# Optimization experiments

Measured on AMD Instinct MI355X. Metric: run time of the kernel, lower is better.

Reference implementation:

```python
import jax, jax.numpy as jnp
import numpy as np
from jax import lax

PATCH = 11          # patch_size
DIL = 2             # dilation_patch
PAD = (PATCH // 2) * DIL  # 10
EPS = 1e-5


def setup_inputs() -> dict:
    key = jax.random.key(0)
    k0, k1, kw, kb, kg, kbe = jax.random.split(key, 6)
    B, C, H, W = 8, 128, 192, 192
    x0 = jax.random.normal(k0, (B, C, H, W), dtype=jnp.float32)
    x1 = jax.random.normal(k1, (B, C, H, W), dtype=jnp.float32)
    # Conv2d(121, 8, k=3, s=1, p=1) params + BatchNorm2d(8) affine params
    conv_w = jax.random.normal(kw, (8, 121, 3, 3), dtype=jnp.float32) * 0.05
    conv_b = jax.random.normal(kb, (8,), dtype=jnp.float32) * 0.05
    gamma = jnp.ones((8,), dtype=jnp.float32)
    beta = jnp.zeros((8,), dtype=jnp.float32)
    return {"x0": x0, "x1": x1, "conv_w": conv_w, "conv_b": conv_b,
            "gamma": gamma, "beta": beta}


def _correlation(x0, x1):
    """spatial_correlation_sample(kernel=1, patch=11, stride=1, pad=0, dil_patch=2).
    out[b, pi*11+pj, i, j] = sum_c x0[b,c,i,j] * x1[b,c, i+(pi-5)*2, j+(pj-5)*2]
    (zero-padded outside)."""
    x1p = jnp.pad(x1, ((0, 0), (0, 0), (PAD, PAD), (PAD, PAD)))
    slices = []
    for pi in range(PATCH):       # static 11x11 displacement grid
        for pj in range(PATCH):
            x1s = lax.dynamic_slice(x1p, (0, 0, pi * DIL, pj * DIL), x1.shape)
            slices.append(jnp.einsum('bchw,bchw->bhw', x0, x1s))
    return jnp.stack(slices, axis=1)  # [B, 121, H, W]


def reference(x0, x1, conv_w, conv_b, gamma, beta):
    y = _correlation(x0, x1)  # [B, 121, H, W]
    y = lax.conv_general_dilated(y, conv_w, window_strides=(1, 1),
                                 padding=((1, 1), (1, 1)),
                                 dimension_numbers=('NCHW', 'OIHW', 'NCHW'))
    y = y + conv_b[None, :, None, None]
    # BatchNorm2d in training mode: batch statistics over (B, H, W), biased var
    mean = jnp.mean(y, axis=(0, 2, 3))
    var = jnp.var(y, axis=(0, 2, 3))
    y = (y - mean[None, :, None, None]) * (gamma / jnp.sqrt(var + EPS))[None, :, None, None] \
        + beta[None, :, None, None]
    return jax.nn.relu(y)
```

## Files before the change

kernel.cpp:

```cpp
#include <hip/hip_runtime.h>

#define HH 192
#define WW 192
#define CC 128
#define BB 8
#define HW (HH * WW)
#define OC 8
#define NPIX (BB * HW)

typedef __attribute__((ext_vector_type(8))) short bf16x8;
typedef __attribute__((ext_vector_type(4))) float f32x4;

__device__ __forceinline__ unsigned short f2bf(float f) {
    unsigned int u = __float_as_uint(f);
    u += 0x7fffu + ((u >> 16) & 1u);
    return (unsigned short)(u >> 16);
}
__device__ __forceinline__ float bf2f(unsigned short u) {
    return __uint_as_float(((unsigned int)u) << 16);
}

__global__ __launch_bounds__(256) void k_transpose(
    const float* __restrict__ x0, const float* __restrict__ x1,
    unsigned short* __restrict__ ws)
{
    const int h = blockIdx.x, b = blockIdx.y, t = blockIdx.z;
    const float* src = t ? x1 : x0;
    unsigned short* dst = ws + (size_t)t * ((size_t)BB * HH * WW * CC);
    __shared__ unsigned short lds[WW * 130];

    for (int idx = threadIdx.x; idx < CC * WW; idx += 256) {
        const int w = idx % WW, c = idx / WW;
        const float v = src[((size_t)(b * CC + c) * HH + h) * WW + w];
        lds[w * 130 + c] = f2bf(v);
    }
    __syncthreads();
    unsigned int* dw = (unsigned int*)(dst + (size_t)(b * HH + h) * WW * CC);
    for (int idx = threadIdx.x; idx < WW * (CC / 2); idx += 256) {
        const int w = idx / (CC / 2), cp = idx % (CC / 2);
        const unsigned int lo = lds[w * 130 + 2 * cp];
        const unsigned int hi = lds[w * 130 + 2 * cp + 1];
        dw[w * (CC / 2) + cp] = lo | (hi << 16);
    }
}

__global__ __launch_bounds__(384, 3) void k_corr_mfma_conv(
    const unsigned short* __restrict__ x0t, const unsigned short* __restrict__ x1t,
    const float* __restrict__ cw, const float* __restrict__ cb,
    float* __restrict__ y)
{
    const int b    = blockIdx.y;
    const int i0   = blockIdx.x * 6;
    const int tid  = threadIdx.x;
    const int wave = tid >> 6, lane = tid & 63;
    const int ln15 = lane & 15, kg = lane >> 4;

    __shared__ unsigned short corr[8][194][11];

    if (tid < 176) {
        const int ir = tid / 22, rem = tid % 22;
        const int pj = rem % 11, jj = (rem < 11) ? 0 : 193;
        corr[ir][jj][pj] = 0;
    }

    float yacc[3][OC];
#pragma unroll
    for (int k = 0; k < 3; ++k)
#pragma unroll
        for (int o = 0; o < OC; ++o) yacc[k][o] = 0.f;

    const int jt  = tid % 192;
    const int irb = tid / 192;

    const bf16x8 zf = {0,0,0,0,0,0,0,0};

    for (int pi = 0; pi < 11; ++pi) {
        __syncthreads();

        for (int g = wave; g < 96; g += 6) {
            const int ir  = g / 12, rem = g % 12;
            const int par = rem / 6, ut = rem % 6;
            const int u0  = ut * 16;
            const int i   = i0 - 1 + ir;
            const bool iv = (i >= 0) && (i < HH);
            const int r   = i + 2 * pi - 10;
            const bool rv = iv && (r >= 0) && (r < HH);
            const int icl = iv ? i : 0;
            const int rcl = rv ? r : 0;

            const unsigned short* pa =
                x0t + ((size_t)((b * HH + icl) * WW + (2 * (u0 + ln15) + par)) * CC + kg * 8);
            bf16x8 a0, a1, a2, a3;
            if (iv) {
                a0 = *(const bf16x8*)(pa);
                a1 = *(const bf16x8*)(pa + 32);
                a2 = *(const bf16x8*)(pa + 64);
                a3 = *(const bf16x8*)(pa + 96);
            } else { a0 = a1 = a2 = a3 = zf; }

#pragma unroll
            for (int vt = 0; vt < 2; ++vt) {
                const int v0 = u0 - 8 + vt * 16;
                const int v  = v0 + ln15;
                const bool vv = rv && (v >= 0) && (v < 96);
                const int vcl = (v < 0) ? 0 : (v > 95 ? 95 : v);
                const unsigned short* pb =
                    x1t + ((size_t)((b * HH + rcl) * WW + (2 * vcl + par)) * CC + kg * 8);
                bf16x8 b0 = *(const bf16x8*)(pb);
                bf16x8 b1 = *(const bf16x8*)(pb + 32);
                bf16x8 b2 = *(const bf16x8*)(pb + 64);
                bf16x8 b3 = *(const bf16x8*)(pb + 96);
                if (!vv) { b0 = zf; b1 = zf; b2 = zf; b3 = zf; }

                f32x4 c = {0.f, 0.f, 0.f, 0.f};
                c = __builtin_amdgcn_mfma_f32_16x16x32_bf16(a0, b0, c, 0, 0, 0);
                c = __builtin_amdgcn_mfma_f32_16x16x32_bf16(a1, b1, c, 0, 0, 0);
                c = __builtin_amdgcn_mfma_f32_16x16x32_bf16(a2, b2, c, 0, 0, 0);
                c = __builtin_amdgcn_mfma_f32_16x16x32_bf16(a3, b3, c, 0, 0, 0);

#pragma unroll
                for (int reg = 0; reg < 4; ++reg) {
                    const int u  = u0 + kg * 4 + reg;
                    const int pj = v0 + ln15 - u + 5;
                    if (pj >= 0 && pj < 11)
                        corr[ir][2 * u + par + 1][pj] = f2bf(c[reg]);
                }
            }
        }
        __syncthreads();

        for (int ki = 0; ki < 3; ++ki) {
            for (int kj = 0; kj < 3; ++kj) {
                float cv[3][11];
#pragma unroll
                for (int k = 0; k < 3; ++k) {
                    const unsigned short* cp = &corr[irb + 2 * k + ki][jt + kj][0];
#pragma unroll
                    for (int pj = 0; pj < 11; ++pj) cv[k][pj] = bf2f(cp[pj]);
                }
#pragma unroll
                for (int o = 0; o < OC; ++o) {
                    float y0 = yacc[0][o], y1 = yacc[1][o], y2 = yacc[2][o];
#pragma unroll
                    for (int pj = 0; pj < 11; ++pj) {
                        const float wv =
                            cw[(((o * 121) + pi * 11 + pj) * 3 + ki) * 3 + kj];
                        y0 = fmaf(wv, cv[0][pj], y0);
                        y1 = fmaf(wv, cv[1][pj], y1);
                        y2 = fmaf(wv, cv[2][pj], y2);
                    }
                    yacc[0][o] = y0; yacc[1][o] = y1; yacc[2][o] = y2;
                }
            }
        }
    }

#pragma unroll
    for (int k = 0; k < 3; ++k) {
        const int irow = i0 + irb + 2 * k;
#pragma unroll
        for (int o = 0; o < OC; ++o)
            y[((size_t)(b * OC + o) * HH + irow) * WW + jt] = yacc[k][o] + cb[o];
    }
}

__global__ __launch_bounds__(256) void k_corr_conv(
    const float* __restrict__ x0, const float* __restrict__ x1,
    const float* __restrict__ cw, const float* __restrict__ cb,
    float* __restrict__ y)
{
    const int b  = blockIdx.z;
    const int i0 = blockIdx.y * 14;
    const int j0 = blockIdx.x * 14;
    const int li = threadIdx.x >> 4;
    const int lj = threadIdx.x & 15;
    const int gi = i0 + li - 1;
    const int gj = j0 + lj - 1;
    const bool valid    = (gi >= 0) & (gi < HH) & (gj >= 0) & (gj < WW);
    const bool interior = (li >= 1) & (li <= 14) & (lj >= 1) & (lj <= 14)
                        & (gi < HH) & (gj < WW);

    __shared__ float corr[16][16][13];

    float yacc[OC];
#pragma unroll
    for (int o = 0; o < OC; ++o) yacc[o] = 0.f;

    const size_t bbase = (size_t)b * CC * HW;
    const float* x0p = x0 + bbase + (size_t)gi * WW + gj;

    for (int pi = 0; pi < 11; ++pi) {
        float acc[11];
#pragma unroll
        for (int k = 0; k < 11; ++k) acc[k] = 0.f;

        const int r = gi + 2 * pi - 10;
        if (valid && r >= 0 && r < HH) {
            const float* p0 = x0p;
            if (gj >= 10 && gj <= WW - 11) {
                const float* p1o = x1 + bbase + (size_t)r * WW + (gj - 10);
#pragma unroll 2
                for (int c = 0; c < CC; ++c) {
                    const float a = *p0;
#pragma unroll
                    for (int k = 0; k < 11; ++k)
                        acc[k] = fmaf(a, p1o[2 * k], acc[k]);
                    p0 += HW; p1o += HW;
                }
            } else {
                const float* p1 = x1 + bbase + (size_t)r * WW;
#pragma unroll 2
                for (int c = 0; c < CC; ++c) {
                    const float a = *p0;
#pragma unroll
                    for (int k = 0; k < 11; ++k) {
                        const int col = gj + 2 * k - 10;
                        const float v = (col >= 0 && col < WW) ? p1[col] : 0.f;
                        acc[k] = fmaf(a, v, acc[k]);
                    }
                    p0 += HW; p1 += HW;
                }
            }
        }

        __syncthreads();
#pragma unroll
        for (int k = 0; k < 11; ++k) corr[li][lj][k] = acc[k];
        __syncthreads();

        if (interior) {
#pragma unroll
            for (int ki = 0; ki < 3; ++ki) {
#pragma unroll
                for (int kj = 0; kj < 3; ++kj) {
                    float cv[11];
#pragma unroll
                    for (int k = 0; k < 11; ++k)
                        cv[k] = corr[li + ki - 1][lj + kj - 1][k];
#pragma unroll
                    for (int o = 0; o < OC; ++o) {
#pragma unroll
                        for (int k = 0; k < 11; ++k) {
                            const float wv =
                                cw[(((o * 121) + pi * 11 + k) * 3 + ki) * 3 + kj];
                            yacc[o] = fmaf(wv, cv[k], yacc[o]);
                        }
                    }
                }
            }
        }
    }

    if (interior) {
#pragma unroll
        for (int o = 0; o < OC; ++o)
            y[(size_t)(b * OC + o) * HW + (size_t)gi * WW + gj] = yacc[o] + cb[o];
    }
}

__global__ __launch_bounds__(256) void k_stats_partial(
    const float* __restrict__ y, float* __restrict__ ws)
{
    const int o = blockIdx.x & 7;
    const int b = blockIdx.x >> 3;
    const float4* p = (const float4*)(y + (size_t)(b * OC + o) * HW);
    float s = 0.f, q = 0.f;
    for (int t = threadIdx.x; t < HW / 4; t += 256) {
        const float4 v = p[t];
        s += v.x + v.y + v.z + v.w;
        q = fmaf(v.x, v.x, q); q = fmaf(v.y, v.y, q);
        q = fmaf(v.z, v.z, q); q = fmaf(v.w, v.w, q);
    }
#pragma unroll
    for (int off = 32; off > 0; off >>= 1) {
        s += __shfl_down(s, off);
        q += __shfl_down(q, off);
    }
    __shared__ float ss[4], sq[4];
    const int lane = threadIdx.x & 63, wv = threadIdx.x >> 6;
    if (lane == 0) { ss[wv] = s; sq[wv] = q; }
    __syncthreads();
    if (threadIdx.x == 0) {
        ws[blockIdx.x]      = ss[0] + ss[1] + ss[2] + ss[3];
        ws[64 + blockIdx.x] = sq[0] + sq[1] + sq[2] + sq[3];
    }
}

__global__ void k_stats_final(float* __restrict__ ws,
                              const float* __restrict__ gamma,
                              const float* __restrict__ beta)
{
    const int o = threadIdx.x;
    if (o < 8) {
        float S = 0.f, Q = 0.f;
#pragma unroll
        for (int b = 0; b < 8; ++b) {
            S += ws[b * 8 + o];
            Q += ws[64 + b * 8 + o];
        }
        const float invN = 1.f / (float)NPIX;
        const float mean = S * invN;
        const float var  = Q * invN - mean * mean;
        const float sc   = gamma[o] / sqrtf(var + 1e-5f);
        ws[128 + o] = sc;
        ws[136 + o] = beta[o] - mean * sc;
    }
}

__global__ __launch_bounds__(256) void k_bn_relu(
    float* __restrict__ y, const float* __restrict__ ws)
{
    const int i = blockIdx.x * 256 + threadIdx.x;
    const int o = (i / (HW / 4)) & 7;
    const float sc = ws[128 + o], sh = ws[136 + o];
    float4 v = ((float4*)y)[i];
    v.x = fmaxf(fmaf(v.x, sc, sh), 0.f);
    v.y = fmaxf(fmaf(v.y, sc, sh), 0.f);
    v.z = fmaxf(fmaf(v.z, sc, sh), 0.f);
    v.w = fmaxf(fmaf(v.w, sc, sh), 0.f);
    ((float4*)y)[i] = v;
}

extern "C" void kernel_launch(void* const* d_in, const int* in_sizes, int n_in,
                              void* d_out, int out_size, void* d_ws, size_t ws_size,
                              hipStream_t stream)
{
    const float* x0    = (const float*)d_in[0];
    const float* x1    = (const float*)d_in[1];
    const float* cw    = (const float*)d_in[2];
    const float* cb    = (const float*)d_in[3];
    const float* gamma = (const float*)d_in[4];
    const float* beta  = (const float*)d_in[5];
    float* y  = (float*)d_out;
    float* ws = (float*)d_ws;

    const size_t need = (size_t)2 * BB * HH * WW * CC * sizeof(unsigned short);

    if (ws_size >= need) {
        unsigned short* x0t = (unsigned short*)d_ws;
        unsigned short* x1t = x0t + (size_t)BB * HH * WW * CC;
        k_transpose<<<dim3(HH, BB, 2), 256, 0, stream>>>(x0, x1, (unsigned short*)d_ws);
        k_corr_mfma_conv<<<dim3(32, BB), 384, 0, stream>>>(x0t, x1t, cw, cb, y);
    } else {
        dim3 g1(14, 14, 8);
        k_corr_conv<<<g1, 256, 0, stream>>>(x0, x1, cw, cb, y);
    }
    k_stats_partial<<<64, 256, 0, stream>>>(y, ws);
    k_stats_final<<<1, 64, 0, stream>>>(ws, gamma, beta);
    k_bn_relu<<<(OC * BB * HW / 4) / 256, 256, 0, stream>>>(y, ws);
}
```

Before: 611.7 us.

## Shrink correlation-conv tiles to two output rows per block and keep fp32 LDS

The fused correlation+conv kernel now has each block produce 2 output rows instead of 6, giving 768 blocks interleaved across batch instead of 256. The LDS correlation buffer is stored as fp32 rather than bf16, and out-of-range rows and columns are zeroed at the LDS store instead of on the loaded operands, so loads are clamped and unconditional. The aim is better CU occupancy and fewer idle waves, at the cost of more halo recomputation: 4 correlation rows are computed per 2 output rows, versus 8 per 6 before.

```diff
diff --git a/kernel.cpp b/kernel.cpp
--- a/kernel.cpp
+++ b/kernel.cpp
@@ -16,9 +16,6 @@
     u += 0x7fffu + ((u >> 16) & 1u);
     return (unsigned short)(u >> 16);
 }
-__device__ __forceinline__ float bf2f(unsigned short u) {
-    return __uint_as_float(((unsigned int)u) << 16);
-}
 
 __global__ __launch_bounds__(256) void k_transpose(
     const float* __restrict__ x0, const float* __restrict__ x1,
@@ -49,68 +46,59 @@
     const float* __restrict__ cw, const float* __restrict__ cb,
     float* __restrict__ y)
 {
-    const int b    = blockIdx.y;
-    const int i0   = blockIdx.x * 6;
+    const int bid  = blockIdx.x;
+    const int b    = bid & 7;
+    const int i0   = (bid >> 3) * 2;
     const int tid  = threadIdx.x;
     const int wave = tid >> 6, lane = tid & 63;
     const int ln15 = lane & 15, kg = lane >> 4;
 
-    __shared__ unsigned short corr[8][194][11];
-
-    if (tid < 176) {
+    __shared__ float corr[4][194][11];
+
+    if (tid < 88) {
         const int ir = tid / 22, rem = tid % 22;
         const int pj = rem % 11, jj = (rem < 11) ? 0 : 193;
-        corr[ir][jj][pj] = 0;
-    }
-
-    float yacc[3][OC];
-#pragma unroll
-    for (int k = 0; k < 3; ++k)
-#pragma unroll
-        for (int o = 0; o < OC; ++o) yacc[k][o] = 0.f;
-
-    const int jt  = tid % 192;
-    const int irb = tid / 192;
-
-    const bf16x8 zf = {0,0,0,0,0,0,0,0};
+        corr[ir][jj][pj] = 0.f;
+    }
+
+    float yacc[OC];
+#pragma unroll
+    for (int o = 0; o < OC; ++o) yacc[o] = 0.f;
+
+    const int oi = tid / 192;
+    const int jt = tid % 192;
 
     for (int pi = 0; pi < 11; ++pi) {
         __syncthreads();
 
-        for (int g = wave; g < 96; g += 6) {
+        for (int g = wave; g < 48; g += 6) {
             const int ir  = g / 12, rem = g % 12;
             const int par = rem / 6, ut = rem % 6;
             const int u0  = ut * 16;
             const int i   = i0 - 1 + ir;
-            const bool iv = (i >= 0) && (i < HH);
             const int r   = i + 2 * pi - 10;
-            const bool rv = iv && (r >= 0) && (r < HH);
-            const int icl = iv ? i : 0;
-            const int rcl = rv ? r : 0;
+            const bool gv = (i >= 0) && (i < HH) && (r >= 0) && (r < HH);
+            const int icl = min(max(i, 0), HH - 1);
+            const int rcl = min(max(r, 0), HH - 1);
 
             const unsigned short* pa =
                 x0t + ((size_t)((b * HH + icl) * WW + (2 * (u0 + ln15) + par)) * CC + kg * 8);
-            bf16x8 a0, a1, a2, a3;
-            if (iv) {
-                a0 = *(const bf16x8*)(pa);
-                a1 = *(const bf16x8*)(pa + 32);
-                a2 = *(const bf16x8*)(pa + 64);
-                a3 = *(const bf16x8*)(pa + 96);
-            } else { a0 = a1 = a2 = a3 = zf; }
+            const bf16x8 a0 = *(const bf16x8*)(pa);
+            const bf16x8 a1 = *(const bf16x8*)(pa + 32);
+            const bf16x8 a2 = *(const bf16x8*)(pa + 64);
+            const bf16x8 a3 = *(const bf16x8*)(pa + 96);
 
 #pragma unroll
             for (int vt = 0; vt < 2; ++vt) {
-                const int v0 = u0 - 8 + vt * 16;
-                const int v  = v0 + ln15;
-                const bool vv = rv && (v >= 0) && (v < 96);
-                const int vcl = (v < 0) ? 0 : (v > 95 ? 95 : v);
+                const int v0  = u0 - 8 + vt * 16;
+                const int v   = v0 + ln15;
+                const int vcl = min(max(v, 0), 95);
                 const unsigned short* pb =
                     x1t + ((size_t)((b * HH + rcl) * WW + (2 * vcl + par)) * CC + kg * 8);
-                bf16x8 b0 = *(const bf16x8*)(pb);
-                bf16x8 b1 = *(const bf16x8*)(pb + 32);
-                bf16x8 b2 = *(const bf16x8*)(pb + 64);
-                bf16x8 b3 = *(const bf16x8*)(pb + 96);
-                if (!vv) { b0 = zf; b1 = zf; b2 = zf; b3 = zf; }
+                const bf16x8 b0 = *(const bf16x8*)(pb);
+                const bf16x8 b1 = *(const bf16x8*)(pb + 32);
+                const bf16x8 b2 = *(const bf16x8*)(pb + 64);
+                const bf16x8 b3 = *(const bf16x8*)(pb + 96);
 
                 f32x4 c = {0.f, 0.f, 0.f, 0.f};
                 c = __builtin_amdgcn_mfma_f32_16x16x32_bf16(a0, b0, c, 0, 0, 0);
@@ -118,12 +106,13 @@
                 c = __builtin_amdgcn_mfma_f32_16x16x32_bf16(a2, b2, c, 0, 0, 0);
                 c = __builtin_amdgcn_mfma_f32_16x16x32_bf16(a3, b3, c, 0, 0, 0);
 
+                const bool lv = gv && (v >= 0) && (v < 96);
 #pragma unroll
                 for (int reg = 0; reg < 4; ++reg) {
                     const int u  = u0 + kg * 4 + reg;
-                    const int pj = v0 + ln15 - u + 5;
+                    const int pj = v - u + 5;
                     if (pj >= 0 && pj < 11)
-                        corr[ir][2 * u + par + 1][pj] = f2bf(c[reg]);
+                        corr[ir][2 * u + par + 1][pj] = lv ? c[reg] : 0.f;
                 }
             }
         }
@@ -131,37 +120,29 @@
 
         for (int ki = 0; ki < 3; ++ki) {
             for (int kj = 0; kj < 3; ++kj) {
-                float cv[3][11];
-#pragma unroll
-                for (int k = 0; k < 3; ++k) {
-                    const unsigned short* cp = &corr[irb + 2 * k + ki][jt + kj][0];
-#pragma unroll
-                    for (int pj = 0; pj < 11; ++pj) cv[k][pj] = bf2f(cp[pj]);
-                }
+                const float* cp = &corr[oi + ki][jt + kj][0];
+                float cv[11];
+#pragma unroll
+                for (int pj = 0; pj < 11; ++pj) cv[pj] = cp[pj];
 #pragma unroll
                 for (int o = 0; o < OC; ++o) {
-                    float y0 = yacc[0][o], y1 = yacc[1][o], y2 = yacc[2][o];
+                    float acc = yacc[o];
 #pragma unroll
                     for (int pj = 0; pj < 11; ++pj) {
                         const float wv =
                             cw[(((o * 121) + pi * 11 + pj) * 3 + ki) * 3 + kj];
-                        y0 = fmaf(wv, cv[0][pj], y0);
-                        y1 = fmaf(wv, cv[1][pj], y1);
-                        y2 = fmaf(wv, cv[2][pj], y2);
+                        acc = fmaf(wv, cv[pj], acc);
                     }
-                    yacc[0][o] = y0; yacc[1][o] = y1; yacc[2][o] = y2;
+                    yacc[o] = acc;
                 }
             }
         }
     }
 
-#pragma unroll
-    for (int k = 0; k < 3; ++k) {
-        const int irow = i0 + irb + 2 * k;
-#pragma unroll
-        for (int o = 0; o < OC; ++o)
-            y[((size_t)(b * OC + o) * HH + irow) * WW + jt] = yacc[k][o] + cb[o];
-    }
+    const int irow = i0 + oi;
+#pragma unroll
+    for (int o = 0; o < OC; ++o)
+        y[((size_t)(b * OC + o) * HH + irow) * WW + jt] = yacc[o] + cb[o];
 }
 
 __global__ __launch_bounds__(256) void k_corr_conv(
@@ -340,7 +321,7 @@
         unsigned short* x0t = (unsigned short*)d_ws;
         unsigned short* x1t = x0t + (size_t)BB * HH * WW * CC;
         k_transpose<<<dim3(HH, BB, 2), 256, 0, stream>>>(x0, x1, (unsigned short*)d_ws);
-        k_corr_mfma_conv<<<dim3(32, BB), 384, 0, stream>>>(x0t, x1t, cw, cb, y);
+        k_corr_mfma_conv<<<768, 384, 0, stream>>>(x0t, x1t, cw, cb, y);
     } else {
         dim3 g1(14, 14, 8);
         k_corr_conv<<<g1, 256, 0, stream>>>(x0, x1, cw, cb, y);
```

Result: slower. 706.7 us (+15.5%).

## Software-pipeline MFMA fragment loads and store correlation tile in fp32 LDS

Applied to the files above, without the earlier changes.

Restructures the correlation stage so each wave owns a fixed column tile and double-buffers its bf16 fragment loads, prefetching the next row/parity (and next pi) while issuing MFMAs for the current one. Boundary handling moves from zeroing loaded fragments to masking the stored results. The LDS correlation tile becomes fp32, which removes bf16 round-trips but doubles LDS use and may reduce resident blocks per CU. The batch-norm stats reduction is also split over four times as many blocks.

```diff
diff --git a/kernel.cpp b/kernel.cpp
--- a/kernel.cpp
+++ b/kernel.cpp
@@ -16,9 +16,6 @@
     u += 0x7fffu + ((u >> 16) & 1u);
     return (unsigned short)(u >> 16);
 }
-__device__ __forceinline__ float bf2f(unsigned short u) {
-    return __uint_as_float(((unsigned int)u) << 16);
-}
 
 __global__ __launch_bounds__(256) void k_transpose(
     const float* __restrict__ x0, const float* __restrict__ x1,
@@ -44,6 +41,67 @@
     }
 }
 
+__device__ __forceinline__ void load_frags(
+    bf16x8 (&fa)[4], bf16x8 (&fb)[2][4],
+    const unsigned short* __restrict__ x0b, const unsigned short* __restrict__ x1b,
+    int i0, int u0, int ln15, int kg, int pi, int s)
+{
+    const int ir = s >> 1, par = s & 1;
+    const int i  = i0 - 1 + ir;
+    const int r  = i + 2 * pi - 10;
+    const int icl = min(max(i, 0), HH - 1);
+    const int rcl = min(max(r, 0), HH - 1);
+
+    const unsigned short* pa =
+        x0b + ((size_t)(icl * WW + (2 * (u0 + ln15) + par))) * CC + kg * 8;
+    fa[0] = *(const bf16x8*)(pa);
+    fa[1] = *(const bf16x8*)(pa + 32);
+    fa[2] = *(const bf16x8*)(pa + 64);
+    fa[3] = *(const bf16x8*)(pa + 96);
+
+#pragma unroll
+    for (int vt = 0; vt < 2; ++vt) {
+        const int v   = u0 - 8 + vt * 16 + ln15;
+        const int vcl = min(max(v, 0), 95);
+        const unsigned short* pb =
+            x1b + ((size_t)(rcl * WW + (2 * vcl + par))) * CC + kg * 8;
+        fb[vt][0] = *(const bf16x8*)(pb);
+        fb[vt][1] = *(const bf16x8*)(pb + 32);
+        fb[vt][2] = *(const bf16x8*)(pb + 64);
+        fb[vt][3] = *(const bf16x8*)(pb + 96);
+    }
+}
+
+__device__ __forceinline__ void consume_frags(
+    const bf16x8 (&fa)[4], const bf16x8 (&fb)[2][4],
+    float (&corr)[8][194][11],
+    int i0, int u0, int ln15, int kg, int pi, int s)
+{
+    const int ir = s >> 1, par = s & 1;
+    const int i  = i0 - 1 + ir;
+    const int r  = i + 2 * pi - 10;
+    const bool gv = (i >= 0) && (i < HH) && (r >= 0) && (r < HH);
+
+#pragma unroll
+    for (int vt = 0; vt < 2; ++vt) {
+        f32x4 c = {0.f, 0.f, 0.f, 0.f};
+        c = __builtin_amdgcn_mfma_f32_16x16x32_bf16(fa[0], fb[vt][0], c, 0, 0, 0);
+        c = __builtin_amdgcn_mfma_f32_16x16x32_bf16(fa[1], fb[vt][1], c, 0, 0, 0);
+        c = __builtin_amdgcn_mfma_f32_16x16x32_bf16(fa[2], fb[vt][2], c, 0, 0, 0);
+        c = __builtin_amdgcn_mfma_f32_16x16x32_bf16(fa[3], fb[vt][3], c, 0, 0, 0);
+
+        const int v  = u0 - 8 + vt * 16 + ln15;
+        const bool lv = gv && (v >= 0) && (v < 96);
+#pragma unroll
+        for (int rg = 0; rg < 4; ++rg) {
+            const int u  = u0 + kg * 4 + rg;
+            const int pj = v - u + 5;
+            if (pj >= 0 && pj < 11)
+                corr[ir][2 * u + par + 1][pj] = lv ? c[rg] : 0.f;
+        }
+    }
+}
+
 __global__ __launch_bounds__(384, 3) void k_corr_mfma_conv(
     const unsigned short* __restrict__ x0t, const unsigned short* __restrict__ x1t,
     const float* __restrict__ cw, const float* __restrict__ cb,
@@ -54,13 +112,14 @@
     const int tid  = threadIdx.x;
     const int wave = tid >> 6, lane = tid & 63;
     const int ln15 = lane & 15, kg = lane >> 4;
-
-    __shared__ unsigned short corr[8][194][11];
+    const int u0   = wave * 16;
+
+    __shared__ float corr[8][194][11];
 
     if (tid < 176) {
         const int ir = tid / 22, rem = tid % 22;
         const int pj = rem % 11, jj = (rem < 11) ? 0 : 193;
-        corr[ir][jj][pj] = 0;
+        corr[ir][jj][pj] = 0.f;
     }
 
     float yacc[3][OC];
@@ -72,60 +131,27 @@
     const int jt  = tid % 192;
     const int irb = tid / 192;
 
-    const bf16x8 zf = {0,0,0,0,0,0,0,0};
+    const size_t ibase = (size_t)b * HH * WW * CC;
+    const unsigned short* x0b = x0t + ibase;
+    const unsigned short* x1b = x1t + ibase;
+
+    bf16x8 fa0[4], fa1[4];
+    bf16x8 fb0[2][4], fb1[2][4];
+
+    load_frags(fa0, fb0, x0b, x1b, i0, u0, ln15, kg, 0, 0);
 
     for (int pi = 0; pi < 11; ++pi) {
         __syncthreads();
 
-        for (int g = wave; g < 96; g += 6) {
-            const int ir  = g / 12, rem = g % 12;
-            const int par = rem / 6, ut = rem % 6;
-            const int u0  = ut * 16;
-            const int i   = i0 - 1 + ir;
-            const bool iv = (i >= 0) && (i < HH);
-            const int r   = i + 2 * pi - 10;
-            const bool rv = iv && (r >= 0) && (r < HH);
-            const int icl = iv ? i : 0;
-            const int rcl = rv ? r : 0;
-
-            const unsigned short* pa =
-                x0t + ((size_t)((b * HH + icl) * WW + (2 * (u0 + ln15) + par)) * CC + kg * 8);
-            bf16x8 a0, a1, a2, a3;
-            if (iv) {
-                a0 = *(const bf16x8*)(pa);
-                a1 = *(const bf16x8*)(pa + 32);
-                a2 = *(const bf16x8*)(pa + 64);
-                a3 = *(const bf16x8*)(pa + 96);
-            } else { a0 = a1 = a2 = a3 = zf; }
-
-#pragma unroll
-            for (int vt = 0; vt < 2; ++vt) {
-                const int v0 = u0 - 8 + vt * 16;
-                const int v  = v0 + ln15;
-                const bool vv = rv && (v >= 0) && (v < 96);
-                const int vcl = (v < 0) ? 0 : (v > 95 ? 95 : v);
-                const unsigned short* pb =
-                    x1t + ((size_t)((b * HH + rcl) * WW + (2 * vcl + par)) * CC + kg * 8);
-                bf16x8 b0 = *(const bf16x8*)(pb);
-                bf16x8 b1 = *(const bf16x8*)(pb + 32);
-                bf16x8 b2 = *(const bf16x8*)(pb + 64);
-                bf16x8 b3 = *(const bf16x8*)(pb + 96);
-                if (!vv) { b0 = zf; b1 = zf; b2 = zf; b3 = zf; }
-
-                f32x4 c = {0.f, 0.f, 0.f, 0.f};
-                c = __builtin_amdgcn_mfma_f32_16x16x32_bf16(a0, b0, c, 0, 0, 0);
-                c = __builtin_amdgcn_mfma_f32_16x16x32_bf16(a1, b1, c, 0, 0, 0);
-                c = __builtin_amdgcn_mfma_f32_16x16x32_bf16(a2, b2, c, 0, 0, 0);
-                c = __builtin_amdgcn_mfma_f32_16x16x32_bf16(a3, b3, c, 0, 0, 0);
-
-#pragma unroll
-                for (int reg = 0; reg < 4; ++reg) {
-                    const int u  = u0 + kg * 4 + reg;
-                    const int pj = v0 + ln15 - u + 5;
-                    if (pj >= 0 && pj < 11)
-                        corr[ir][2 * u + par + 1][pj] = f2bf(c[reg]);
-                }
-            }
+#pragma unroll
+        for (int sp = 0; sp < 8; ++sp) {
+            const int s0 = 2 * sp, s1 = 2 * sp + 1;
+            load_frags(fa1, fb1, x0b, x1b, i0, u0, ln15, kg, pi, s1);
+            consume_frags(fa0, fb0, corr, i0, u0, ln15, kg, pi, s0);
+            const int pin = (sp == 7) ? min(pi + 1, 10) : pi;
+            const int s2  = (sp == 7) ? 0 : s1 + 1;
+            load_frags(fa0, fb0, x0b, x1b, i0, u0, ln15, kg, pin, s2);
+            consume_frags(fa1, fb1, corr, i0, u0, ln15, kg, pi, s1);
         }
         __syncthreads();
 
@@ -134,9 +160,9 @@
                 float cv[3][11];
 #pragma unroll
                 for (int k = 0; k < 3; ++k) {
-                    const unsigned short* cp = &corr[irb + 2 * k + ki][jt + kj][0];
-#pragma unroll
-                    for (int pj = 0; pj < 11; ++pj) cv[k][pj] = bf2f(cp[pj]);
+                    const float* cp = &corr[irb + 2 * k + ki][jt + kj][0];
+#pragma unroll
+                    for (int pj = 0; pj < 11; ++pj) cv[k][pj] = cp[pj];
                 }
 #pragma unroll
                 for (int o = 0; o < OC; ++o) {
@@ -144,7 +170,7 @@
 #pragma unroll
                     for (int pj = 0; pj < 11; ++pj) {
                         const float wv =
-                            cw[(((o * 121) + pi * 11 + pj) * 3 + ki) * 3 + kj];
+                            cw[o * 1089 + (pi * 11 + pj) * 9 + ki * 3 + kj];
                         y0 = fmaf(wv, cv[0][pj], y0);
                         y1 = fmaf(wv, cv[1][pj], y1);
                         y2 = fmaf(wv, cv[2][pj], y2);
@@ -261,28 +287,29 @@
 __global__ __launch_bounds__(256) void k_stats_partial(
     const float* __restrict__ y, float* __restrict__ ws)
 {
-    const int o = blockIdx.x & 7;
-    const int b = blockIdx.x >> 3;
-    const float4* p = (const float4*)(y + (size_t)(b * OC + o) * HW);
-    float s = 0.f, q = 0.f;
-    for (int t = threadIdx.x; t < HW / 4; t += 256) {
+    const int bid = blockIdx.x;
+    const int b = bid >> 5, rem = bid & 31;
+    const int o = rem >> 2, q = rem & 3;
+    const float4* p = (const float4*)(y + (size_t)(b * OC + o) * HW) + q * (HW / 16);
+    float s = 0.f, qq = 0.f;
+    for (int t = threadIdx.x; t < HW / 16; t += 256) {
         const float4 v = p[t];
         s += v.x + v.y + v.z + v.w;
-        q = fmaf(v.x, v.x, q); q = fmaf(v.y, v.y, q);
-        q = fmaf(v.z, v.z, q); q = fmaf(v.w, v.w, q);
+        qq = fmaf(v.x, v.x, qq); qq = fmaf(v.y, v.y, qq);
+        qq = fmaf(v.z, v.z, qq); qq = fmaf(v.w, v.w, qq);
     }
 #pragma unroll
     for (int off = 32; off > 0; off >>= 1) {
-        s += __shfl_down(s, off);
-        q += __shfl_down(q, off);
+        s  += __shfl_down(s, off);
+        qq += __shfl_down(qq, off);
     }
     __shared__ float ss[4], sq[4];
     const int lane = threadIdx.x & 63, wv = threadIdx.x >> 6;
-    if (lane == 0) { ss[wv] = s; sq[wv] = q; }
+    if (lane == 0) { ss[wv] = s; sq[wv] = qq; }
     __syncthreads();
     if (threadIdx.x == 0) {
-        ws[blockIdx.x]      = ss[0] + ss[1] + ss[2] + ss[3];
-        ws[64 + blockIdx.x] = sq[0] + sq[1] + sq[2] + sq[3];
+        ws[bid]       = ss[0] + ss[1] + ss[2] + ss[3];
+        ws[256 + bid] = sq[0] + sq[1] + sq[2] + sq[3];
     }
 }
 
@@ -294,16 +321,18 @@
     if (o < 8) {
         float S = 0.f, Q = 0.f;
 #pragma unroll
-        for (int b = 0; b < 8; ++b) {
-            S += ws[b * 8 + o];
-            Q += ws[64 + b * 8 + o];
-        }
+        for (int b = 0; b < 8; ++b)
+#pragma unroll
+            for (int q = 0; q < 4; ++q) {
+                S += ws[b * 32 + o * 4 + q];
+                Q += ws[256 + b * 32 + o * 4 + q];
+            }
         const float invN = 1.f / (float)NPIX;
         const float mean = S * invN;
         const float var  = Q * invN - mean * mean;
         const float sc   = gamma[o] / sqrtf(var + 1e-5f);
-        ws[128 + o] = sc;
-        ws[136 + o] = beta[o] - mean * sc;
+        ws[512 + o] = sc;
+        ws[520 + o] = beta[o] - mean * sc;
     }
 }
 
@@ -312,7 +341,7 @@
 {
     const int i = blockIdx.x * 256 + threadIdx.x;
     const int o = (i / (HW / 4)) & 7;
-    const float sc = ws[128 + o], sh = ws[136 + o];
+    const float sc = ws[512 + o], sh = ws[520 + o];
     float4 v = ((float4*)y)[i];
     v.x = fmaxf(fmaf(v.x, sc, sh), 0.f);
     v.y = fmaxf(fmaf(v.y, sc, sh), 0.f);
@@ -345,7 +374,7 @@
         dim3 g1(14, 14, 8);
         k_corr_conv<<<g1, 256, 0, stream>>>(x0, x1, cw, cb, y);
     }
-    k_stats_partial<<<64, 256, 0, stream>>>(y, ws);
+    k_stats_partial<<<256, 256, 0, stream>>>(y, ws);
     k_stats_final<<<1, 64, 0, stream>>>(ws, gamma, beta);
     k_bn_relu<<<(OC * BB * HW / 4) / 256, 256, 0, stream>>>(y, ws);
 }
```

New measurement: 804.9 us. +31.6%, slower.

## Split correlation-conv kernel over displacement rows into partial sums for more blocks

Applied to the files above, without the earlier changes.

The fused correlation+conv kernel now divides the 11 displacement rows (pi) across up to four parts chosen from spare workspace. Each part writes its own partial output buffer, which raises the grid from 256 blocks to up to 1024 and adds an XCD-aware block index swizzle. The stats and BN/ReLU kernels sum the partial buffers while reading, and the stats kernel uses more blocks. The aim is better occupancy and load balance on the many-CU GPU, at the cost of extra global memory traffic for the partial buffers and dropping the occupancy hint from launch bounds.

```diff
diff --git a/kernel.cpp b/kernel.cpp
--- a/kernel.cpp
+++ b/kernel.cpp
@@ -7,6 +7,7 @@
 #define HW (HH * WW)
 #define OC 8
 #define NPIX (BB * HW)
+#define YCHUNK (OC * BB * HW)
 
 typedef __attribute__((ext_vector_type(8))) short bf16x8;
 typedef __attribute__((ext_vector_type(4))) float f32x4;
@@ -44,13 +45,22 @@
     }
 }
 
-__global__ __launch_bounds__(384, 3) void k_corr_mfma_conv(
+__global__ __launch_bounds__(384) void k_corr_mfma_conv(
     const unsigned short* __restrict__ x0t, const unsigned short* __restrict__ x1t,
     const float* __restrict__ cw, const float* __restrict__ cb,
-    float* __restrict__ y)
-{
-    const int b    = blockIdx.y;
-    const int i0   = blockIdx.x * 6;
+    float* __restrict__ yparts, int split)
+{
+    const int N = 256 * split;
+    const int L = blockIdx.x;
+    const int w = (L & 7) * (N >> 3) + (L >> 3);
+    const int b     = w / (32 * split);
+    const int rem   = w % (32 * split);
+    const int part  = rem >> 5;
+    const int strip = rem & 31;
+    const int i0    = strip * 6;
+    const int plo   = (11 * part) / split;
+    const int phi   = (11 * (part + 1)) / split;
+
     const int tid  = threadIdx.x;
     const int wave = tid >> 6, lane = tid & 63;
     const int ln15 = lane & 15, kg = lane >> 4;
@@ -58,8 +68,8 @@
     __shared__ unsigned short corr[8][194][11];
 
     if (tid < 176) {
-        const int ir = tid / 22, rem = tid % 22;
-        const int pj = rem % 11, jj = (rem < 11) ? 0 : 193;
+        const int ir = tid / 22, rr = tid % 22;
+        const int pj = rr % 11, jj = (rr < 11) ? 0 : 193;
         corr[ir][jj][pj] = 0;
     }
 
@@ -72,45 +82,41 @@
     const int jt  = tid % 192;
     const int irb = tid / 192;
 
-    const bf16x8 zf = {0,0,0,0,0,0,0,0};
-
-    for (int pi = 0; pi < 11; ++pi) {
+    const size_t ibase = (size_t)b * HH * WW * CC;
+    const unsigned short* x0b = x0t + ibase;
+    const unsigned short* x1b = x1t + ibase;
+
+    for (int pi = plo; pi < phi; ++pi) {
         __syncthreads();
 
         for (int g = wave; g < 96; g += 6) {
-            const int ir  = g / 12, rem = g % 12;
-            const int par = rem / 6, ut = rem % 6;
+            const int ir  = g / 12, rr = g % 12;
+            const int par = rr / 6, ut = rr % 6;
             const int u0  = ut * 16;
             const int i   = i0 - 1 + ir;
-            const bool iv = (i >= 0) && (i < HH);
             const int r   = i + 2 * pi - 10;
-            const bool rv = iv && (r >= 0) && (r < HH);
-            const int icl = iv ? i : 0;
-            const int rcl = rv ? r : 0;
+            const bool gv = (i >= 0) && (i < HH) && (r >= 0) && (r < HH);
+            const int icl = min(max(i, 0), HH - 1);
+            const int rcl = min(max(r, 0), HH - 1);
 
             const unsigned short* pa =
-                x0t + ((size_t)((b * HH + icl) * WW + (2 * (u0 + ln15) + par)) * CC + kg * 8);
-            bf16x8 a0, a1, a2, a3;
-            if (iv) {
-                a0 = *(const bf16x8*)(pa);
-                a1 = *(const bf16x8*)(pa + 32);
-                a2 = *(const bf16x8*)(pa + 64);
-                a3 = *(const bf16x8*)(pa + 96);
-            } else { a0 = a1 = a2 = a3 = zf; }
+                x0b + ((size_t)(icl * WW + (2 * (u0 + ln15) + par))) * CC + kg * 8;
+            const bf16x8 a0 = *(const bf16x8*)(pa);
+            const bf16x8 a1 = *(const bf16x8*)(pa + 32);
+            const bf16x8 a2 = *(const bf16x8*)(pa + 64);
+            const bf16x8 a3 = *(const bf16x8*)(pa + 96);
 
 #pragma unroll
             for (int vt = 0; vt < 2; ++vt) {
-                const int v0 = u0 - 8 + vt * 16;
-                const int v  = v0 + ln15;
-                const bool vv = rv && (v >= 0) && (v < 96);
-                const int vcl = (v < 0) ? 0 : (v > 95 ? 95 : v);
+                const int v0  = u0 - 8 + vt * 16;
+                const int v   = v0 + ln15;
+                const int vcl = min(max(v, 0), 95);
                 const unsigned short* pb =
-                    x1t + ((size_t)((b * HH + rcl) * WW + (2 * vcl + par)) * CC + kg * 8);
-                bf16x8 b0 = *(const bf16x8*)(pb);
-                bf16x8 b1 = *(const bf16x8*)(pb + 32);
-                bf16x8 b2 = *(const bf16x8*)(pb + 64);
-                bf16x8 b3 = *(const bf16x8*)(pb + 96);
-                if (!vv) { b0 = zf; b1 = zf; b2 = zf; b3 = zf; }
+                    x1b + ((size_t)(rcl * WW + (2 * vcl + par))) * CC + kg * 8;
+                const bf16x8 b0 = *(const bf16x8*)(pb);
+                const bf16x8 b1 = *(const bf16x8*)(pb + 32);
+                const bf16x8 b2 = *(const bf16x8*)(pb + 64);
+                const bf16x8 b3 = *(const bf16x8*)(pb + 96);
 
                 f32x4 c = {0.f, 0.f, 0.f, 0.f};
                 c = __builtin_amdgcn_mfma_f32_16x16x32_bf16(a0, b0, c, 0, 0, 0);
@@ -118,12 +124,13 @@
                 c = __builtin_amdgcn_mfma_f32_16x16x32_bf16(a2, b2, c, 0, 0, 0);
                 c = __builtin_amdgcn_mfma_f32_16x16x32_bf16(a3, b3, c, 0, 0, 0);
 
-#pragma unroll
-                for (int reg = 0; reg < 4; ++reg) {
-                    const int u  = u0 + kg * 4 + reg;
-                    const int pj = v0 + ln15 - u + 5;
+                const bool lv = gv && (v >= 0) && (v < 96);
+#pragma unroll
+                for (int rg = 0; rg < 4; ++rg) {
+                    const int u  = u0 + kg * 4 + rg;
+                    const int pj = v - u + 5;
                     if (pj >= 0 && pj < 11)
-                        corr[ir][2 * u + par + 1][pj] = f2bf(c[reg]);
+                        corr[ir][2 * u + par + 1][pj] = f2bf(lv ? c[rg] : 0.f);
                 }
             }
         }
@@ -155,12 +162,16 @@
         }
     }
 
+    float* yp = yparts + (size_t)part * YCHUNK;
 #pragma unroll
     for (int k = 0; k < 3; ++k) {
         const int irow = i0 + irb + 2 * k;
 #pragma unroll
-        for (int o = 0; o < OC; ++o)
-            y[((size_t)(b * OC + o) * HH + irow) * WW + jt] = yacc[k][o] + cb[o];
+        for (int o = 0; o < OC; ++o) {
+            float val = yacc[k][o];
+            if (part == 0) val += cb[o];
+            yp[((size_t)(b * OC + o) * HH + irow) * WW + jt] = val;
+        }
     }
 }
 
@@ -259,34 +270,40 @@
 }
 
 __global__ __launch_bounds__(256) void k_stats_partial(
-    const float* __restrict__ y, float* __restrict__ ws)
-{
-    const int o = blockIdx.x & 7;
-    const int b = blockIdx.x >> 3;
-    const float4* p = (const float4*)(y + (size_t)(b * OC + o) * HW);
-    float s = 0.f, q = 0.f;
-    for (int t = threadIdx.x; t < HW / 4; t += 256) {
-        const float4 v = p[t];
-        s += v.x + v.y + v.z + v.w;
-        q = fmaf(v.x, v.x, q); q = fmaf(v.y, v.y, q);
-        q = fmaf(v.z, v.z, q); q = fmaf(v.w, v.w, q);
+    const float* __restrict__ yparts, int split, float* __restrict__ st)
+{
+    const int bid = blockIdx.x;
+    const int b = bid >> 5, rem = bid & 31;
+    const int o = rem >> 2, q = rem & 3;
+    const float4* p = (const float4*)(yparts + (size_t)(b * OC + o) * HW)
+                    + q * (HW / 16);
+    float s = 0.f, qq = 0.f;
+    for (int t = threadIdx.x; t < HW / 16; t += 256) {
+        float4 z = p[t];
+        for (int pp = 1; pp < split; ++pp) {
+            const float4 v = p[t + (size_t)pp * (YCHUNK / 4)];
+            z.x += v.x; z.y += v.y; z.z += v.z; z.w += v.w;
+        }
+        s += z.x + z.y + z.z + z.w;
+        qq = fmaf(z.x, z.x, qq); qq = fmaf(z.y, z.y, qq);
+        qq = fmaf(z.z, z.z, qq); qq = fmaf(z.w, z.w, qq);
     }
 #pragma unroll
     for (int off = 32; off > 0; off >>= 1) {
-        s += __shfl_down(s, off);
-        q += __shfl_down(q, off);
+        s  += __shfl_down(s, off);
+        qq += __shfl_down(qq, off);
     }
     __shared__ float ss[4], sq[4];
     const int lane = threadIdx.x & 63, wv = threadIdx.x >> 6;
-    if (lane == 0) { ss[wv] = s; sq[wv] = q; }
+    if (lane == 0) { ss[wv] = s; sq[wv] = qq; }
     __syncthreads();
     if (threadIdx.x == 0) {
-        ws[blockIdx.x]      = ss[0] + ss[1] + ss[2] + ss[3];
-        ws[64 + blockIdx.x] = sq[0] + sq[1] + sq[2] + sq[3];
-    }
-}
-
-__global__ void k_stats_final(float* __restrict__ ws,
+        st[bid]       = ss[0] + ss[1] + ss[2] + ss[3];
+        st[256 + bid] = sq[0] + sq[1] + sq[2] + sq[3];
+    }
+}
+
+__global__ void k_stats_final(float* __restrict__ st,
                               const float* __restrict__ gamma,
                               const float* __restrict__ beta)
 {
@@ -294,31 +311,40 @@
     if (o < 8) {
         float S = 0.f, Q = 0.f;
 #pragma unroll
-        for (int b = 0; b < 8; ++b) {
-            S += ws[b * 8 + o];
-            Q += ws[64 + b * 8 + o];
-        }
+        for (int b = 0; b < 8; ++b)
+#pragma unroll
+            for (int q = 0; q < 4; ++q) {
+                S += st[b * 32 + o * 4 + q];
+                Q += st[256 + b * 32 + o * 4 + q];
+            }
         const float invN = 1.f / (float)NPIX;
         const float mean = S * invN;
         const float var  = Q * invN - mean * mean;
         const float sc   = gamma[o] / sqrtf(var + 1e-5f);
-        ws[128 + o] = sc;
-        ws[136 + o] = beta[o] - mean * sc;
+        st[512 + o] = sc;
+        st[520 + o] = beta[o] - mean * sc;
     }
 }
 
 __global__ __launch_bounds__(256) void k_bn_relu(
-    float* __restrict__ y, const float* __restrict__ ws)
+    const float* __restrict__ yparts, int split,
+    const float* __restrict__ st, float* __restrict__ out)
 {
     const int i = blockIdx.x * 256 + threadIdx.x;
     const int o = (i / (HW / 4)) & 7;
-    const float sc = ws[128 + o], sh = ws[136 + o];
-    float4 v = ((float4*)y)[i];
-    v.x = fmaxf(fmaf(v.x, sc, sh), 0.f);
-    v.y = fmaxf(fmaf(v.y, sc, sh), 0.f);
-    v.z = fmaxf(fmaf(v.z, sc, sh), 0.f);
-    v.w = fmaxf(fmaf(v.w, sc, sh), 0.f);
-    ((float4*)y)[i] = v;
+    const float sc = st[512 + o], sh = st[520 + o];
+    const float4* p = (const float4*)yparts;
+    float4 z = p[i];
+    for (int pp = 1; pp < split; ++pp) {
+        const float4 v = p[i + (size_t)pp * (YCHUNK / 4)];
+        z.x += v.x; z.y += v.y; z.z += v.z; z.w += v.w;
+    }
+    float4 r;
+    r.x = fmaxf(fmaf(z.x, sc, sh), 0.f);
+    r.y = fmaxf(fmaf(z.y, sc, sh), 0.f);
+    r.z = fmaxf(fmaf(z.z, sc, sh), 0.f);
+    r.w = fmaxf(fmaf(z.w, sc, sh), 0.f);
+    ((float4*)out)[i] = r;
 }
 
 extern "C" void kernel_launch(void* const* d_in, const int* in_sizes, int n_in,
@@ -331,21 +357,32 @@
     const float* cb    = (const float*)d_in[3];
     const float* gamma = (const float*)d_in[4];
     const float* beta  = (const float*)d_in[5];
-    float* y  = (float*)d_out;
-    float* ws = (float*)d_ws;
-
-    const size_t need = (size_t)2 * BB * HH * WW * CC * sizeof(unsigned short);
-
-    if (ws_size >= need) {
+    float* out = (float*)d_out;
+    float* st  = (float*)d_ws;
+
+    const size_t needT  = (size_t)2 * BB * HH * WW * CC * sizeof(unsigned short);
+    const size_t ybytes = (size_t)YCHUNK * sizeof(float);
+
+    if (ws_size >= needT) {
         unsigned short* x0t = (unsigned short*)d_ws;
         unsigned short* x1t = x0t + (size_t)BB * HH * WW * CC;
+
+        int split = (int)((ws_size - needT) / ybytes);
+        if (split > 4) split = 4;
+        float* yparts = (split >= 2) ? (float*)((char*)d_ws + needT) : out;
+        if (split < 1) split = 1;
+
         k_transpose<<<dim3(HH, BB, 2), 256, 0, stream>>>(x0, x1, (unsigned short*)d_ws);
-        k_corr_mfma_conv<<<dim3(32, BB), 384, 0, stream>>>(x0t, x1t, cw, cb, y);
+        k_corr_mfma_conv<<<256 * split, 384, 0, stream>>>(x0t, x1t, cw, cb,
+                                                          yparts, split);
+        k_stats_partial<<<256, 256, 0, stream>>>(yparts, split, st);
+        k_stats_final<<<1, 64, 0, stream>>>(st, gamma, beta);
+        k_bn_relu<<<(YCHUNK / 4) / 256, 256, 0, stream>>>(yparts, split, st, out);
     } else {
         dim3 g1(14, 14, 8);
-        k_corr_conv<<<g1, 256, 0, stream>>>(x0, x1, cw, cb, y);
-    }
-    k_stats_partial<<<64, 256, 0, stream>>>(y, ws);
-    k_stats_final<<<1, 64, 0, stream>>>(ws, gamma, beta);
-    k_bn_relu<<<(OC * BB * HW / 4) / 256, 256, 0, stream>>>(y, ws);
-}
+        k_corr_conv<<<g1, 256, 0, stream>>>(x0, x1, cw, cb, out);
+        k_stats_partial<<<256, 256, 0, stream>>>(out, 1, st);
+        k_stats_final<<<1, 64, 0, stream>>>(st, gamma, beta);
+        k_bn_relu<<<(YCHUNK / 4) / 256, 256, 0, stream>>>(out, 1, st, out);
+    }
+}
```

Result: slower. 655.4 us (+7.1%).
